# Performance work log

Hardware: AMD Instinct MI355X
Metric: run time of the kernel (lower is better)

Reference implementation:

```python
import jax, jax.numpy as jnp
import numpy as np
from jax import lax

RADIUS = 2
KS = 2 * RADIUS + 1            # soft-detect kernel size (5)
TOP_K = 4096                   # static keypoint budget (top_k>0 branch)
TEMP = 0.1                     # softmax temperature


def setup_inputs():
    key = jax.random.key(0)
    scores_map = jax.random.uniform(key, (8, 1, 512, 640), dtype=jnp.float32)
    return {"scores_map": scores_map}


def _max_pool(x):
    # torch max_pool2d(kernel=KS, stride=1, padding=RADIUS) == SAME max pooling
    return lax.reduce_window(x, -jnp.inf, lax.max,
                             (1, 1, KS, KS), (1, 1, 1, 1), 'SAME')


def _simple_nms(scores):
    zeros = jnp.zeros_like(scores)
    max_mask = scores == _max_pool(scores)
    for _ in range(2):
        supp_mask = _max_pool(max_mask.astype(scores.dtype)) > 0
        supp_scores = jnp.where(supp_mask, zeros, scores)
        new_max = supp_scores == _max_pool(supp_scores)
        max_mask = max_mask | (new_max & ~supp_mask)
    return jnp.where(max_mask, scores, zeros)


def _bilinear_sample(img, xy, H, W):
    # img: [B,H,W]; xy: [B,N,2] normalized to [-1,1]; align_corners=True
    px = (xy[..., 0] + 1.0) * 0.5 * (W - 1)
    py = (xy[..., 1] + 1.0) * 0.5 * (H - 1)
    x0 = jnp.floor(px); y0 = jnp.floor(py)
    wx = px - x0; wy = py - y0
    x0i = jnp.clip(x0, 0, W - 1).astype(jnp.int32)
    x1i = jnp.clip(x0 + 1, 0, W - 1).astype(jnp.int32)
    y0i = jnp.clip(y0, 0, H - 1).astype(jnp.int32)
    y1i = jnp.clip(y0 + 1, 0, H - 1).astype(jnp.int32)
    flat = img.reshape(img.shape[0], H * W)
    def take(yy, xx):
        return jnp.take_along_axis(flat, yy * W + xx, axis=1)
    v00 = take(y0i, x0i); v01 = take(y0i, x1i)
    v10 = take(y1i, x0i); v11 = take(y1i, x1i)
    return (v00 * (1 - wx) * (1 - wy) + v01 * wx * (1 - wy)
            + v10 * (1 - wx) * wy + v11 * wx * wy)


def reference(scores_map):
    B, _, H, W = scores_map.shape
    dt = scores_map.dtype
    r = RADIUS

    # --- NMS on detached scores ---
    s_ng = lax.stop_gradient(scores_map)
    nms = _simple_nms(s_ng)
    nms = (nms.at[:, :, :r + 1, :].set(0.)
              .at[:, :, :, :r + 1].set(0.)
              .at[:, :, H - r:, :].set(0.)
              .at[:, :, :, W - r:].set(0.))

    # --- static top-k keypoint selection ---
    _, idx = lax.top_k(nms.reshape(B, -1), TOP_K)          # [B,N] int32

    # --- unfold: gather KSxKS patches (zero padded), torch Unfold layout (kh outer, kw inner) ---
    sp = jnp.pad(scores_map[:, 0], ((0, 0), (r, r), (r, r)))
    patches = jnp.stack([sp[:, di:di + H, dj:dj + W]
                         for di in range(KS) for dj in range(KS)], axis=1)  # [B,25,H,W]
    patches = patches.reshape(B, KS * KS, H * W).transpose(0, 2, 1)          # [B,HW,25]
    ps = jnp.take_along_axis(patches, idx[:, :, None], axis=1)              # [B,N,25]

    # hw_grid: rows are (dx, dy), dx inner-varying -- matches torch meshgrid 'ij' + [:, [1,0]]
    x = jnp.linspace(-r, r, KS, dtype=dt)
    gy, gx = jnp.meshgrid(x, x, indexing='ij')
    hw_grid = jnp.stack([gx.ravel(), gy.ravel()], axis=-1)                   # [25,2]

    # --- temperature softmax soft-argmax ---
    max_v = lax.stop_gradient(ps.max(axis=-1, keepdims=True))
    x_exp = jnp.exp((ps - max_v) / TEMP)                                     # [B,N,25]
    ssum = x_exp.sum(axis=-1, keepdims=True)
    xy_res = jnp.einsum('bnp,pc->bnc', x_exp, hw_grid) / ssum                # [B,N,2]
    d2 = jnp.sum(((hw_grid[None, None] - xy_res[:, :, None, :]) / r) ** 2, axis=-1)
    disp = (x_exp * d2).sum(axis=-1) / ssum[..., 0]                          # [B,N]

    kxy_nms = jnp.stack([idx % W, idx // W], axis=-1).astype(dt)             # [B,N,2]
    kxy = kxy_nms + xy_res
    kxy = kxy / jnp.array([W - 1, H - 1], dtype=dt) * 2.0 - 1.0              # normalized

    kptscore = _bilinear_sample(scores_map[:, 0], kxy, H, W)                 # [B,N]
    return kxy, kptscore, disp
```

## Files before the change

### kernel.cpp

```cpp
#include <hip/hip_runtime.h>
#include <cstdint>

#define BN 8
#define HH 512
#define WW 640
#define HWp (HH*WW)
#define NPIX (BN*HWp)
#define RAD 2
#define TOPK 4096
#define NBINS 65536
#define CAND_CAP 8192

#define OFF_M     0
#define OFF_U     (OFF_M + NPIX)
#define OFF_HIST  (OFF_U + NPIX)
#define OFF_CNT   (OFF_HIST + BN*NBINS*4)
#define OFF_TBIN  (OFF_CNT + 1024)
#define OFF_CAND  (OFF_TBIN + 128)
#define OFF_KPIDX (OFF_CAND + BN*CAND_CAP*8)

#define CNT_STRIDE 32

#define TILE 32
#define HALO 10
#define STG  52
#define LSTR 56
#define GTX  20
#define GTY  16

__global__ void k_zero(unsigned* __restrict__ p, int n) {
    int i = blockIdx.x * blockDim.x + threadIdx.x;
    if (i < n) p[i] = 0u;
}

__global__ __launch_bounds__(256) void k_nms_fused(const float* __restrict__ S,
                                                   uint8_t* __restrict__ M,
                                                   unsigned* __restrict__ hist) {
    __shared__ float   sm [STG][LSTR];
    __shared__ float   tmp[STG][LSTR];
    __shared__ uint8_t mbuf[STG][LSTR];
    __shared__ uint8_t ubuf[STG][LSTR];

    int bid = blockIdx.x;
    int b   = bid / (GTX * GTY);
    int t   = bid - b * (GTX * GTY);
    int tyy = t / GTX, txx = t - tyy * GTX;
    int oy = tyy * TILE - HALO;
    int ox = txx * TILE - HALO;
    const float* img = S + b * HWp;
    int tid = threadIdx.x;
    const float NEG = -__builtin_inff();

    for (int idx = tid; idx < STG * STG; idx += 256) {
        int i = idx / STG, j = idx - i * STG;
        int Y = oy + i, X = ox + j;
        sm[i][j] = (Y >= 0 && Y < HH && X >= 0 && X < WW) ? img[Y * WW + X] : NEG;
    }
    __syncthreads();

    for (int idx = tid; idx < 48 * STG; idx += 256) {
        int r = idx / STG, j = idx - r * STG;
        int ci = r + 2;
        float m0 = fmaxf(fmaxf(sm[ci-2][j], sm[ci-1][j]),
                         fmaxf(sm[ci][j],   sm[ci+1][j]));
        tmp[ci][j] = fmaxf(m0, sm[ci+2][j]);
    }
    __syncthreads();
    for (int idx = tid; idx < 48 * 48; idx += 256) {
        int r = idx / 48, c = idx - r * 48;
        int ci = r + 2, cj = c + 2;
        float mx = fmaxf(fmaxf(tmp[ci][cj-2], tmp[ci][cj-1]),
                         fmaxf(fmaxf(tmp[ci][cj], tmp[ci][cj+1]), tmp[ci][cj+2]));
        int Y = oy + ci, X = ox + cj;
        bool valid = (Y >= 0 && Y < HH && X >= 0 && X < WW);
        mbuf[ci][cj] = (valid && sm[ci][cj] == mx) ? (uint8_t)1 : (uint8_t)0;
    }
    __syncthreads();

    for (int idx = tid; idx < 44 * STG; idx += 256) {
        int r = idx / STG, j = idx - r * STG;
        int ci = r + 4;
        int acc = mbuf[ci-2][j] | mbuf[ci-1][j] | mbuf[ci][j]
                | mbuf[ci+1][j] | mbuf[ci+2][j];
        tmp[ci][j] = (float)acc;
    }
    __syncthreads();
    for (int idx = tid; idx < 44 * 44; idx += 256) {
        int r = idx / 44, c = idx - r * 44;
        int ci = r + 4, cj = c + 4;
        float mx = fmaxf(fmaxf(tmp[ci][cj-2], tmp[ci][cj-1]),
                         fmaxf(fmaxf(tmp[ci][cj], tmp[ci][cj+1]), tmp[ci][cj+2]));
        ubuf[ci][cj] = (mx > 0.f) ? (uint8_t)1 : (uint8_t)0;
    }
    __syncthreads();

    for (int idx = tid; idx < 40 * STG; idx += 256) {
        int r = idx / STG, j = idx - r * STG;
        int ci = r + 6;
        float v0 = ubuf[ci-2][j] ? 0.f : sm[ci-2][j];
        float v1 = ubuf[ci-1][j] ? 0.f : sm[ci-1][j];
        float v2 = ubuf[ci  ][j] ? 0.f : sm[ci  ][j];
        float v3 = ubuf[ci+1][j] ? 0.f : sm[ci+1][j];
        float v4 = ubuf[ci+2][j] ? 0.f : sm[ci+2][j];
        tmp[ci][j] = fmaxf(fmaxf(fmaxf(v0, v1), fmaxf(v2, v3)), v4);
    }
    __syncthreads();
    for (int idx = tid; idx < 40 * 40; idx += 256) {
        int r = idx / 40, c = idx - r * 40;
        int ci = r + 6, cj = c + 6;
        float mx = fmaxf(fmaxf(tmp[ci][cj-2], tmp[ci][cj-1]),
                         fmaxf(fmaxf(tmp[ci][cj], tmp[ci][cj+1]), tmp[ci][cj+2]));
        uint8_t u = ubuf[ci][cj];
        float vc = u ? 0.f : sm[ci][cj];
        int Y = oy + ci, X = ox + cj;
        bool valid = (Y >= 0 && Y < HH && X >= 0 && X < WW);
        if (valid && !u && vc == mx) mbuf[ci][cj] = 1;
    }
    __syncthreads();

    for (int idx = tid; idx < 36 * STG; idx += 256) {
        int r = idx / STG, j = idx - r * STG;
        int ci = r + 8;
        int acc = mbuf[ci-2][j] | mbuf[ci-1][j] | mbuf[ci][j]
                | mbuf[ci+1][j] | mbuf[ci+2][j];
        tmp[ci][j] = (float)acc;
    }
    __syncthreads();
    for (int idx = tid; idx < 36 * 36; idx += 256) {
        int r = idx / 36, c = idx - r * 36;
        int ci = r + 8, cj = c + 8;
        float mx = fmaxf(fmaxf(tmp[ci][cj-2], tmp[ci][cj-1]),
                         fmaxf(fmaxf(tmp[ci][cj], tmp[ci][cj+1]), tmp[ci][cj+2]));
        ubuf[ci][cj] = (mx > 0.f) ? (uint8_t)1 : (uint8_t)0;
    }
    __syncthreads();

    for (int idx = tid; idx < 32 * STG; idx += 256) {
        int r = idx / STG, j = idx - r * STG;
        int ci = r + 10;
        float v0 = ubuf[ci-2][j] ? 0.f : sm[ci-2][j];
        float v1 = ubuf[ci-1][j] ? 0.f : sm[ci-1][j];
        float v2 = ubuf[ci  ][j] ? 0.f : sm[ci  ][j];
        float v3 = ubuf[ci+1][j] ? 0.f : sm[ci+1][j];
        float v4 = ubuf[ci+2][j] ? 0.f : sm[ci+2][j];
        tmp[ci][j] = fmaxf(fmaxf(fmaxf(v0, v1), fmaxf(v2, v3)), v4);
    }
    __syncthreads();
    for (int idx = tid; idx < 32 * 32; idx += 256) {
        int r = idx >> 5, c = idx & 31;
        int ci = r + 10, cj = c + 10;
        int Y = oy + ci, X = ox + cj;
        if (Y >= HH || X >= WW) continue;
        float mx = fmaxf(fmaxf(tmp[ci][cj-2], tmp[ci][cj-1]),
                         fmaxf(fmaxf(tmp[ci][cj], tmp[ci][cj+1]), tmp[ci][cj+2]));
        uint8_t u = ubuf[ci][cj];
        float cv = sm[ci][cj];
        float vc = u ? 0.f : cv;
        uint8_t m3 = mbuf[ci][cj];
        if (!u && vc == mx) m3 = 1;
        M[b * HWp + Y * WW + X] = m3;
        if (m3 && Y >= RAD + 1 && Y < HH - RAD && X >= RAD + 1 && X < WW - RAD
            && cv != 0.f) {
            unsigned bits = __float_as_uint(cv);
            atomicAdd(&hist[b * NBINS + (bits >> 16)], 1u);
        }
    }
}

__global__ __launch_bounds__(1024) void k_scan(const unsigned* __restrict__ hist,
                                               int* __restrict__ Tbin) {
    __shared__ unsigned b0[1024], b1[1024];
    int b = blockIdx.x, t = threadIdx.x;
    const unsigned* h = hist + b * NBINS;
    int base = NBINS - (t + 1) * 64;
    unsigned s = 0;
    for (int i = 0; i < 64; ++i) s += h[base + i];
    b0[t] = s;
    __syncthreads();
    unsigned* src = b0; unsigned* dst = b1;
    for (int off = 1; off < 1024; off <<= 1) {
        unsigned v = src[t];
        if (t >= off) v += src[t - off];
        dst[t] = v;
        __syncthreads();
        unsigned* tmp2 = src; src = dst; dst = tmp2;
    }
    unsigned incl = src[t];
    unsigned excl = incl - s;
    unsigned total = src[1023];
    const unsigned K = TOPK;
    if (excl < K && K <= incl) {
        unsigned run = excl;
        for (int i = 0; i < 64; ++i) {
            int bin = NBINS - 1 - t * 64 - i;
            unsigned c = h[bin];
            if (run < K && K <= run + c) { Tbin[b] = bin; break; }
            run += c;
        }
    }
    if (t == 1023 && total < K) Tbin[b] = 0;
}

__global__ void k_compact(const float* __restrict__ S, const uint8_t* __restrict__ M,
                          const int* __restrict__ Tbin,
                          unsigned* __restrict__ cnt, unsigned long long* __restrict__ cand) {
    __shared__ unsigned lcnt, lbase;
    int gid = blockIdx.x * 256 + threadIdx.x;
    int b = gid / HWp, p = gid - b * HWp;
    int y = p / WW, x = p - y * WW;
    if (threadIdx.x == 0) lcnt = 0;
    __syncthreads();
    bool win = false;
    unsigned mypos = 0;
    unsigned long long key = 0;
    if (M[gid] && y >= RAD + 1 && y < HH - RAD && x >= RAD + 1 && x < WW - RAD) {
        float v = S[gid];
        if (v != 0.f) {
            unsigned bits = __float_as_uint(v);
            if ((int)(bits >> 16) >= Tbin[b]) {
                mypos = atomicAdd(&lcnt, 1u);
                key = ((unsigned long long)bits << 32) | (unsigned)(~(unsigned)p);
                win = true;
            }
        }
    }
    __syncthreads();
    if (threadIdx.x == 0 && lcnt)
        lbase = atomicAdd(&cnt[b * CNT_STRIDE], lcnt);
    __syncthreads();
    if (win) {
        unsigned pos = lbase + mypos;
        if (pos < CAND_CAP) cand[b * CAND_CAP + pos] = key;
    }
}

__global__ __launch_bounds__(1024) void k_sort(const unsigned* __restrict__ cnt,
                                               const unsigned long long* __restrict__ cand,
                                               int* __restrict__ kp) {
    __shared__ unsigned long long keys[CAND_CAP];
    int b = blockIdx.x, t = threadIdx.x;
    unsigned nr = cnt[b * CNT_STRIDE];
    if (nr > CAND_CAP) nr = CAND_CAP;
    for (int i = t; i < CAND_CAP; i += 1024)
        keys[i] = (i < (int)nr) ? cand[b * CAND_CAP + i] : 0ull;
    __syncthreads();
    for (int k = 2; k <= CAND_CAP; k <<= 1) {
        for (int j = k >> 1; j > 0; j >>= 1) {
            for (int i = t; i < CAND_CAP; i += 1024) {
                int ixj = i ^ j;
                if (ixj > i) {
                    bool asc = (i & k) != 0;
                    unsigned long long a = keys[i], c = keys[ixj];
                    bool sw = asc ? (a > c) : (a < c);
                    if (sw) { keys[i] = c; keys[ixj] = a; }
                }
            }
            __syncthreads();
        }
    }
    for (int i = t; i < TOPK; i += 1024) {
        unsigned long long key = keys[i];
        int idx;
        if (key != 0ull) idx = (int)(~(unsigned)(key & 0xFFFFFFFFull));
        else             idx = i - (int)nr;
        kp[b * TOPK + i] = idx;
    }
}

__global__ void k_kp(const float* __restrict__ S, const int* __restrict__ kp,
                     float* __restrict__ out) {
    int g = blockIdx.x * blockDim.x + threadIdx.x;
    if (g >= BN * TOPK) return;
    int b = g >> 12;
    int idx = kp[g];
    int y = idx / WW, x = idx - y * WW;
    const float* img = S + b * HWp;
    float ps[25];
#pragma unroll
    for (int di = 0; di < 5; ++di) {
#pragma unroll
        for (int dj = 0; dj < 5; ++dj) {
            int yy = y + di - RAD, xx = x + dj - RAD;
            bool ok = (yy >= 0) && (yy < HH) && (xx >= 0) && (xx < WW);
            ps[di * 5 + dj] = ok ? img[yy * WW + xx] : 0.f;
        }
    }
    float mx = ps[0];
#pragma unroll
    for (int p = 1; p < 25; ++p) mx = fmaxf(mx, ps[p]);
    float ssum = 0.f, sx = 0.f, sy = 0.f, sg2 = 0.f;
#pragma unroll
    for (int p = 0; p < 25; ++p) {
        float dx = (float)(p % 5) - 2.f;
        float dy = (float)(p / 5) - 2.f;
        float e = expf((ps[p] - mx) / 0.1f);
        ssum += e;
        sx += e * dx;
        sy += e * dy;
        sg2 += e * (dx * dx + dy * dy);
    }
    float xr = sx / ssum, yr = sy / ssum;
    float disp = (sg2 - 2.f * (xr * sx + yr * sy) + (xr * xr + yr * yr) * ssum)
                 / (4.f * ssum);
    float kxn = ((float)x + xr) / (float)(WW - 1) * 2.f - 1.f;
    float kyn = ((float)y + yr) / (float)(HH - 1) * 2.f - 1.f;
    out[2 * g]     = kxn;
    out[2 * g + 1] = kyn;
    float px = (kxn + 1.f) * 0.5f * (float)(WW - 1);
    float py = (kyn + 1.f) * 0.5f * (float)(HH - 1);
    float x0 = floorf(px), y0f = floorf(py);
    float wx = px - x0, wy = py - y0f;
    int x0i = (int)fminf(fmaxf(x0, 0.f), (float)(WW - 1));
    int x1i = (int)fminf(fmaxf(x0 + 1.f, 0.f), (float)(WW - 1));
    int y0i = (int)fminf(fmaxf(y0f, 0.f), (float)(HH - 1));
    int y1i = (int)fminf(fmaxf(y0f + 1.f, 0.f), (float)(HH - 1));
    float v00 = img[y0i * WW + x0i], v01 = img[y0i * WW + x1i];
    float v10 = img[y1i * WW + x0i], v11 = img[y1i * WW + x1i];
    float sc = v00 * (1.f - wx) * (1.f - wy) + v01 * wx * (1.f - wy)
             + v10 * (1.f - wx) * wy + v11 * wx * wy;
    out[BN * TOPK * 2 + g] = sc;
    out[BN * TOPK * 3 + g] = disp;
}

extern "C" void kernel_launch(void* const* d_in, const int* in_sizes, int n_in,
                              void* d_out, int out_size, void* d_ws, size_t ws_size,
                              hipStream_t stream) {
    const float* S = (const float*)d_in[0];
    float* out = (float*)d_out;
    char* ws = (char*)d_ws;

    uint8_t*            M     = (uint8_t*)(ws + OFF_M);
    unsigned*           hist  = (unsigned*)(ws + OFF_HIST);
    unsigned*           cnt   = (unsigned*)(ws + OFF_CNT);
    int*                Tbin  = (int*)(ws + OFF_TBIN);
    unsigned long long* cand  = (unsigned long long*)(ws + OFF_CAND);
    int*                kpidx = (int*)(ws + OFF_KPIDX);

    int zwords = (BN * NBINS * 4 + 1024) / 4;
    k_zero<<<(zwords + 255) / 256, 256, 0, stream>>>(hist, zwords);

    k_nms_fused<<<BN * GTX * GTY, 256, 0, stream>>>(S, M, hist);

    int nblk = (NPIX + 255) / 256;
    k_scan<<<BN, 1024, 0, stream>>>(hist, Tbin);
    k_compact<<<nblk, 256, 0, stream>>>(S, M, Tbin, cnt, cand);
    k_sort<<<BN, 1024, 0, stream>>>(cnt, cand, kpidx);
    k_kp<<<(BN * TOPK + 255) / 256, 256, 0, stream>>>(S, kpidx, out);
}
```

Measured before the change: 424.8 us.

## Double NMS block size, vectorize scan and compaction, use fast exp

Raises the fused NMS kernel to 512 threads per block and drops a bounds check that the tile geometry makes redundant. Loads histogram bins as uint4 in the scan kernel. Has each compaction thread handle four pixels, reading the mask as one 32-bit word and doing one shared atomic per thread. Replaces expf with __expf and the division by a multiply in the keypoint kernel. Together these aim to cut per-pixel work, atomic traffic and load count, at some risk to register pressure and a small loss of exp precision.

```diff
diff --git a/kernel.cpp b/kernel.cpp
--- a/kernel.cpp
+++ b/kernel.cpp
@@ -27,15 +27,16 @@
 #define LSTR 56
 #define GTX  20
 #define GTY  16
+#define NMS_T 512
 
 __global__ void k_zero(unsigned* __restrict__ p, int n) {
     int i = blockIdx.x * blockDim.x + threadIdx.x;
     if (i < n) p[i] = 0u;
 }
 
-__global__ __launch_bounds__(256) void k_nms_fused(const float* __restrict__ S,
-                                                   uint8_t* __restrict__ M,
-                                                   unsigned* __restrict__ hist) {
+__global__ __launch_bounds__(NMS_T) void k_nms_fused(const float* __restrict__ S,
+                                                     uint8_t* __restrict__ M,
+                                                     unsigned* __restrict__ hist) {
     __shared__ float   sm [STG][LSTR];
     __shared__ float   tmp[STG][LSTR];
     __shared__ uint8_t mbuf[STG][LSTR];
@@ -51,14 +52,14 @@
     int tid = threadIdx.x;
     const float NEG = -__builtin_inff();
 
-    for (int idx = tid; idx < STG * STG; idx += 256) {
+    for (int idx = tid; idx < STG * STG; idx += NMS_T) {
         int i = idx / STG, j = idx - i * STG;
         int Y = oy + i, X = ox + j;
         sm[i][j] = (Y >= 0 && Y < HH && X >= 0 && X < WW) ? img[Y * WW + X] : NEG;
     }
     __syncthreads();
 
-    for (int idx = tid; idx < 48 * STG; idx += 256) {
+    for (int idx = tid; idx < 48 * STG; idx += NMS_T) {
         int r = idx / STG, j = idx - r * STG;
         int ci = r + 2;
         float m0 = fmaxf(fmaxf(sm[ci-2][j], sm[ci-1][j]),
@@ -66,7 +67,7 @@
         tmp[ci][j] = fmaxf(m0, sm[ci+2][j]);
     }
     __syncthreads();
-    for (int idx = tid; idx < 48 * 48; idx += 256) {
+    for (int idx = tid; idx < 48 * 48; idx += NMS_T) {
         int r = idx / 48, c = idx - r * 48;
         int ci = r + 2, cj = c + 2;
         float mx = fmaxf(fmaxf(tmp[ci][cj-2], tmp[ci][cj-1]),
@@ -77,7 +78,7 @@
     }
     __syncthreads();
 
-    for (int idx = tid; idx < 44 * STG; idx += 256) {
+    for (int idx = tid; idx < 44 * STG; idx += NMS_T) {
         int r = idx / STG, j = idx - r * STG;
         int ci = r + 4;
         int acc = mbuf[ci-2][j] | mbuf[ci-1][j] | mbuf[ci][j]
@@ -85,7 +86,7 @@
         tmp[ci][j] = (float)acc;
     }
     __syncthreads();
-    for (int idx = tid; idx < 44 * 44; idx += 256) {
+    for (int idx = tid; idx < 44 * 44; idx += NMS_T) {
         int r = idx / 44, c = idx - r * 44;
         int ci = r + 4, cj = c + 4;
         float mx = fmaxf(fmaxf(tmp[ci][cj-2], tmp[ci][cj-1]),
@@ -94,7 +95,7 @@
     }
     __syncthreads();
 
-    for (int idx = tid; idx < 40 * STG; idx += 256) {
+    for (int idx = tid; idx < 40 * STG; idx += NMS_T) {
         int r = idx / STG, j = idx - r * STG;
         int ci = r + 6;
         float v0 = ubuf[ci-2][j] ? 0.f : sm[ci-2][j];
@@ -105,7 +106,7 @@
         tmp[ci][j] = fmaxf(fmaxf(fmaxf(v0, v1), fmaxf(v2, v3)), v4);
     }
     __syncthreads();
-    for (int idx = tid; idx < 40 * 40; idx += 256) {
+    for (int idx = tid; idx < 40 * 40; idx += NMS_T) {
         int r = idx / 40, c = idx - r * 40;
         int ci = r + 6, cj = c + 6;
         float mx = fmaxf(fmaxf(tmp[ci][cj-2], tmp[ci][cj-1]),
@@ -118,7 +119,7 @@
     }
     __syncthreads();
 
-    for (int idx = tid; idx < 36 * STG; idx += 256) {
+    for (int idx = tid; idx < 36 * STG; idx += NMS_T) {
         int r = idx / STG, j = idx - r * STG;
         int ci = r + 8;
         int acc = mbuf[ci-2][j] | mbuf[ci-1][j] | mbuf[ci][j]
@@ -126,7 +127,7 @@
         tmp[ci][j] = (float)acc;
     }
     __syncthreads();
-    for (int idx = tid; idx < 36 * 36; idx += 256) {
+    for (int idx = tid; idx < 36 * 36; idx += NMS_T) {
         int r = idx / 36, c = idx - r * 36;
         int ci = r + 8, cj = c + 8;
         float mx = fmaxf(fmaxf(tmp[ci][cj-2], tmp[ci][cj-1]),
@@ -135,7 +136,7 @@
     }
     __syncthreads();
 
-    for (int idx = tid; idx < 32 * STG; idx += 256) {
+    for (int idx = tid; idx < 32 * STG; idx += NMS_T) {
         int r = idx / STG, j = idx - r * STG;
         int ci = r + 10;
         float v0 = ubuf[ci-2][j] ? 0.f : sm[ci-2][j];
@@ -146,11 +147,10 @@
         tmp[ci][j] = fmaxf(fmaxf(fmaxf(v0, v1), fmaxf(v2, v3)), v4);
     }
     __syncthreads();
-    for (int idx = tid; idx < 32 * 32; idx += 256) {
+    for (int idx = tid; idx < 32 * 32; idx += NMS_T) {
         int r = idx >> 5, c = idx & 31;
         int ci = r + 10, cj = c + 10;
         int Y = oy + ci, X = ox + cj;
-        if (Y >= HH || X >= WW) continue;
         float mx = fmaxf(fmaxf(tmp[ci][cj-2], tmp[ci][cj-1]),
                          fmaxf(fmaxf(tmp[ci][cj], tmp[ci][cj+1]), tmp[ci][cj+2]));
         uint8_t u = ubuf[ci][cj];
@@ -174,7 +174,12 @@
     const unsigned* h = hist + b * NBINS;
     int base = NBINS - (t + 1) * 64;
     unsigned s = 0;
-    for (int i = 0; i < 64; ++i) s += h[base + i];
+    const uint4* h4 = (const uint4*)(h + base);
+#pragma unroll
+    for (int i = 0; i < 16; ++i) {
+        uint4 v = h4[i];
+        s += v.x + v.y + v.z + v.w;
+    }
     b0[t] = s;
     __syncthreads();
     unsigned* src = b0; unsigned* dst = b1;
@@ -201,36 +206,46 @@
     if (t == 1023 && total < K) Tbin[b] = 0;
 }
 
-__global__ void k_compact(const float* __restrict__ S, const uint8_t* __restrict__ M,
-                          const int* __restrict__ Tbin,
-                          unsigned* __restrict__ cnt, unsigned long long* __restrict__ cand) {
+__global__ void k_compact4(const float* __restrict__ S, const uint8_t* __restrict__ M,
+                           const int* __restrict__ Tbin,
+                           unsigned* __restrict__ cnt, unsigned long long* __restrict__ cand) {
     __shared__ unsigned lcnt, lbase;
-    int gid = blockIdx.x * 256 + threadIdx.x;
-    int b = gid / HWp, p = gid - b * HWp;
-    int y = p / WW, x = p - y * WW;
+    int g = blockIdx.x * 256 + threadIdx.x;
+    int gid4 = g * 4;
+    int b = gid4 / HWp, p = gid4 - b * HWp;
+    int y = p / WW, x0 = p - y * WW;
     if (threadIdx.x == 0) lcnt = 0;
     __syncthreads();
-    bool win = false;
-    unsigned mypos = 0;
-    unsigned long long key = 0;
-    if (M[gid] && y >= RAD + 1 && y < HH - RAD && x >= RAD + 1 && x < WW - RAD) {
-        float v = S[gid];
-        if (v != 0.f) {
-            unsigned bits = __float_as_uint(v);
-            if ((int)(bits >> 16) >= Tbin[b]) {
-                mypos = atomicAdd(&lcnt, 1u);
-                key = ((unsigned long long)bits << 32) | (unsigned)(~(unsigned)p);
-                win = true;
+    unsigned long long mykeys[4];
+    int myn = 0;
+    unsigned mw = *(const unsigned*)(M + gid4);
+    if (mw && y >= RAD + 1 && y < HH - RAD) {
+        int Tb = Tbin[b];
+#pragma unroll
+        for (int i = 0; i < 4; ++i) {
+            if ((mw >> (8 * i)) & 0xFFu) {
+                int x = x0 + i;
+                if (x >= RAD + 1 && x < WW - RAD) {
+                    float v = S[gid4 + i];
+                    if (v != 0.f) {
+                        unsigned bits = __float_as_uint(v);
+                        if ((int)(bits >> 16) >= Tb)
+                            mykeys[myn++] = ((unsigned long long)bits << 32)
+                                          | (unsigned)(~(unsigned)(p + i));
+                    }
+                }
             }
         }
     }
+    unsigned base_l = 0;
+    if (myn) base_l = atomicAdd(&lcnt, (unsigned)myn);
     __syncthreads();
     if (threadIdx.x == 0 && lcnt)
         lbase = atomicAdd(&cnt[b * CNT_STRIDE], lcnt);
     __syncthreads();
-    if (win) {
-        unsigned pos = lbase + mypos;
-        if (pos < CAND_CAP) cand[b * CAND_CAP + pos] = key;
+    for (int i = 0; i < myn; ++i) {
+        unsigned pos = lbase + base_l + (unsigned)i;
+        if (pos < CAND_CAP) cand[b * CAND_CAP + pos] = mykeys[i];
     }
 }
 
@@ -293,7 +308,7 @@
     for (int p = 0; p < 25; ++p) {
         float dx = (float)(p % 5) - 2.f;
         float dy = (float)(p / 5) - 2.f;
-        float e = expf((ps[p] - mx) / 0.1f);
+        float e = __expf((ps[p] - mx) * 10.f);
         ssum += e;
         sx += e * dx;
         sy += e * dy;
@@ -339,11 +354,10 @@
     int zwords = (BN * NBINS * 4 + 1024) / 4;
     k_zero<<<(zwords + 255) / 256, 256, 0, stream>>>(hist, zwords);
 
-    k_nms_fused<<<BN * GTX * GTY, 256, 0, stream>>>(S, M, hist);
-
-    int nblk = (NPIX + 255) / 256;
+    k_nms_fused<<<BN * GTX * GTY, NMS_T, 0, stream>>>(S, M, hist);
+
     k_scan<<<BN, 1024, 0, stream>>>(hist, Tbin);
-    k_compact<<<nblk, 256, 0, stream>>>(S, M, Tbin, cnt, cand);
+    k_compact4<<<NPIX / 4 / 256, 256, 0, stream>>>(S, M, Tbin, cnt, cand);
     k_sort<<<BN, 1024, 0, stream>>>(cnt, cand, kpidx);
     k_kp<<<(BN * TOPK + 255) / 256, 256, 0, stream>>>(S, kpidx, out);
 }
```

Result: faster. 386.0 us (-9.1%).
